# Kernel optimization log

Measured on AMD Instinct MI355X. Metric: run time of the kernel, lower is better.

The kernel has to match this reference:

```python
import jax, jax.numpy as jnp
import numpy as np

N = 50000   # nodes
E = 600000  # edges (avg degree ~12)
R = 8       # num_relations = 2 * n_speakers**2, n_speakers=2
B = 32      # num_bases = args.batch_size
GD, H1, H2 = 128, 128, 128


def setup_inputs() -> dict:
    key = jax.random.key(0)
    ks = jax.random.split(key, 16)
    w = lambda k, shape: jax.random.normal(k, shape, jnp.float32) * 0.05
    return {
        "node_features": jax.random.normal(ks[0], (N, GD), jnp.float32),
        "edge_index": jax.random.randint(ks[1], (2, E), 0, N),
        "edge_norm": jax.random.uniform(ks[2], (E,), jnp.float32),
        "edge_type": jax.random.randint(ks[3], (E,), 0, R),
        "basis": w(ks[4], (B, GD, H1)),
        "comp": w(ks[5], (R, B)),
        "root": w(ks[6], (GD, H1)),
        "bias1": jnp.zeros((H1,), jnp.float32),
        "w_key": w(ks[7], (H1, H2)),
        "b_key": jnp.zeros((H2,), jnp.float32),
        "w_query": w(ks[8], (H1, H2)),
        "b_query": jnp.zeros((H2,), jnp.float32),
        "w_value": w(ks[9], (H1, H2)),
        "b_value": jnp.zeros((H2,), jnp.float32),
        "w_skip": w(ks[10], (H1, H2)),
        "b_skip": jnp.zeros((H2,), jnp.float32),
    }


def reference(node_features, edge_index, edge_norm, edge_type, basis, comp,
              root, bias1, w_key, b_key, w_query, b_query, w_value, b_value,
              w_skip, b_skip):
    n = node_features.shape[0]
    r = comp.shape[0]
    src, dst = edge_index[0], edge_index[1]

    # ---- RGCNConv (basis decomposition, per-relation mean aggregation) ----
    W = jnp.einsum('rb,bio->rio', comp, basis)            # [R, GD, H1]
    xW = jnp.einsum('ni,rio->rno', node_features, W)      # [R, N, H1]
    msg = xW[edge_type, src]                              # [E, H1]
    seg = edge_type * n + dst                             # combined (relation, dst) segment id
    agg = jax.ops.segment_sum(msg, seg, num_segments=r * n).reshape(r, n, -1)
    cnt = jax.ops.segment_sum(jnp.ones(msg.shape[0], jnp.float32), seg,
                              num_segments=r * n).reshape(r, n, 1)
    h = (agg / jnp.maximum(cnt, 1.0)).sum(0) + node_features @ root + bias1

    # ---- ResGatedGraphConv: sigmoid(k_i + q_j) * v_j, sum-aggregated + skip ----
    k = h @ w_key + b_key
    q = h @ w_query + b_query
    v = h @ w_value + b_value
    m = jax.nn.sigmoid(k[dst] + q[src]) * v[src]          # [E, H2]
    out = jax.ops.segment_sum(m, dst, num_segments=n) + h @ w_skip + b_skip
    return out
```

## Files before the change

kernel.cpp:

```cpp
#include <hip/hip_runtime.h>
#include <stdint.h>

#define GD 128
#define H1 128
#define H2 128
#define NBASES 32
#define NREL 8
#define KA 1152

typedef __attribute__((ext_vector_type(8))) short bf16x8;
typedef __attribute__((ext_vector_type(4))) float f32x4;

static inline size_t align256(size_t x){ return (x + 255) & ~(size_t)255; }

__device__ __forceinline__ float bf2f(uint32_t u16){
  union { uint32_t u; float f; } c; c.u = (u16 & 0xffffu) << 16; return c.f;
}
__device__ __forceinline__ unsigned short f2bf(float f){
  union { float f; uint32_t u; } c; c.f = f;
  uint32_t u = c.u;
  u += 0x7fffu + ((u >> 16) & 1u);
  return (unsigned short)(u >> 16);
}
__device__ __forceinline__ uint32_t pkbf(float a, float b){
  union { float f; uint32_t u; } ca, cb; ca.f = a; cb.f = b;
  return __builtin_amdgcn_perm(cb.u + 0x8000u, ca.u + 0x8000u, 0x07060302u);
}

__device__ __forceinline__ void async_copy16(void* lds_dst, const void* gsrc){
  __builtin_amdgcn_global_load_lds(
      (const __attribute__((address_space(1))) uint32_t*)gsrc,
      (__attribute__((address_space(3))) uint32_t*)lds_dst, 16, 0, 0);
}

__global__ void k_prep(const float* __restrict__ comp, const float* __restrict__ basis,
                       const float* __restrict__ root, unsigned short* __restrict__ Bht,
                       const float* __restrict__ wk, const float* __restrict__ wq,
                       const float* __restrict__ wv, const float* __restrict__ wsk,
                       const float* __restrict__ bk, const float* __restrict__ bq,
                       const float* __restrict__ bv, const float* __restrict__ bs,
                       unsigned short* __restrict__ B2t, float* __restrict__ Bb,
                       const float4* __restrict__ x, uint2* __restrict__ xout, int cnt4,
                       const int* __restrict__ edst, const int* __restrict__ etyp,
                       int* __restrict__ cnt, int E, int n){
  const float LOG2E = 1.4426950408889634f;
  int b = blockIdx.x, t = threadIdx.x;
  if (b < 576){
    int idx = b*256 + t;
    int row = idx >> 7, i = idx & 127;
    int r = row >> 7, o = row & 127;
    float v;
    if (r < 8){
      float acc = 0.f;
      #pragma unroll
      for (int bb = 0; bb < NBASES; ++bb)
        acc += comp[r*NBASES + bb] * basis[((size_t)bb*GD + i)*H1 + o];
      v = acc;
    } else {
      v = root[(size_t)i*H1 + o];
    }
    Bht[(size_t)o*KA + r*128 + i] = f2bf(v);
  } else if (b < 576 + 256){
    int idx = (b - 576)*256 + t;
    int c = idx / H1, k = idx % H1;
    const float* w = (c < 128) ? wk : (c < 256) ? wq : (c < 384) ? wv : wsk;
    float val = w[(size_t)k*H2 + (c & 127)];
    if (c < 256) val *= LOG2E;
    B2t[idx] = f2bf(val);
    if (idx < 512){
      const float* bia = (idx < 128) ? bk : (idx < 256) ? bq : (idx < 384) ? bv : bs;
      float bval = bia[idx & 127];
      if (idx < 256) bval *= LOG2E;
      Bb[idx] = bval;
    }
  } else {
    int cb = b - (576 + 256);
    int ncastb = (cnt4 + 255) >> 8;
    if (cb < ncastb){
      int i = cb*256 + t;
      if (i < cnt4){
        float4 v = x[i];
        uint2 o; o.x = pkbf(v.x, v.y); o.y = pkbf(v.z, v.w);
        xout[i] = o;
      }
    } else {
      int e = (cb - ncastb)*256 + t;
      if (e < E) atomicAdd(&cnt[etyp[e]*n + edst[e]], 1);
    }
  }
}

__global__ void k_scanA(const int* __restrict__ deg, int* __restrict__ off,
                        int* __restrict__ btot, int len){
  __shared__ int wsum[16];
  int t = threadIdx.x, lane = t & 63, w = t >> 6;
  int i0 = blockIdx.x*8192 + t*8;
  int v[8];
  if (i0 + 7 < len){
    int4 va = *(const int4*)(deg + i0);
    int4 vb = *(const int4*)(deg + i0 + 4);
    v[0]=va.x; v[1]=va.y; v[2]=va.z; v[3]=va.w;
    v[4]=vb.x; v[5]=vb.y; v[6]=vb.z; v[7]=vb.w;
  } else {
    #pragma unroll
    for (int u = 0; u < 8; ++u) v[u] = (i0+u < len) ? deg[i0+u] : 0;
  }
  int s[8]; s[0] = v[0];
  #pragma unroll
  for (int u = 1; u < 8; ++u) s[u] = s[u-1] + v[u];
  int x = s[7];
  #pragma unroll
  for (int d = 1; d < 64; d <<= 1){
    int u = __shfl_up(x, d, 64);
    if (lane >= d) x += u;
  }
  if (lane == 63) wsum[w] = x;
  __syncthreads();
  if (t < 16){
    int y = wsum[t];
    #pragma unroll
    for (int d = 1; d < 16; d <<= 1){
      int u = __shfl_up(y, d, 16);
      if (t >= d) y += u;
    }
    wsum[t] = y;
  }
  __syncthreads();
  int woff = (w > 0) ? wsum[w-1] : 0;
  int excl = woff + x - s[7];
  #pragma unroll
  for (int u = 0; u < 8; ++u)
    if (i0+u < len) off[i0+u] = excl + s[u] - v[u];
  if (t == 0) btot[blockIdx.x] = wsum[15];
}

__global__ void k_scanB(const int* __restrict__ btot, int* __restrict__ off,
                        int* __restrict__ cursor, int len, int sentinel){
  int t = threadIdx.x, bid = blockIdx.x;
  int add = 0;
  for (int j = 0; j < bid; ++j) add += btot[j];
  int i0 = bid*8192 + t*8;
  #pragma unroll
  for (int u = 0; u < 8; ++u){
    int i = i0 + u;
    if (i < len){ int val = off[i] + add; off[i] = val; cursor[i] = val; }
  }
  if (bid == 0 && t == 0) off[len] = sentinel;
}

__global__ void k_scatter_rd(const int* __restrict__ src, const int* __restrict__ dst,
                             const int* __restrict__ typ, int* __restrict__ cursor,
                             int* __restrict__ pk, int E, int n){
  int e = blockIdx.x*blockDim.x + threadIdx.x;
  if (e >= E) return;
  int pos = atomicAdd(&cursor[typ[e]*n + dst[e]], 1);
  pk[pos] = src[e];
}

__global__ void k_agg(const int* __restrict__ off_rd, const int* __restrict__ pk_rd,
                      const uint32_t* __restrict__ x32, unsigned short* __restrict__ A2,
                      int n, int npad){
  int wid = blockIdx.x*(blockDim.x >> 6) + (threadIdx.x >> 6);
  int lane = threadIdx.x & 63;
  if (wid >= npad) return;
  uint32_t* arow = (uint32_t*)(A2 + (size_t)wid*KA);
  if (wid >= n){
    #pragma unroll
    for (int u = 0; u < 9; ++u) arow[u*64 + lane] = 0u;
    return;
  }
  int r8 = lane & 7;
  int o_r = off_rd[(size_t)r8*n + wid];
  int e_r = off_rd[(size_t)r8*n + wid + 1];
  int c_r = e_r - o_r;
  int c0_ = __builtin_amdgcn_readlane(c_r, 0), c1_ = __builtin_amdgcn_readlane(c_r, 1);
  int c2_ = __builtin_amdgcn_readlane(c_r, 2), c3_ = __builtin_amdgcn_readlane(c_r, 3);
  int c4_ = __builtin_amdgcn_readlane(c_r, 4), c5_ = __builtin_amdgcn_readlane(c_r, 5);
  int c6_ = __builtin_amdgcn_readlane(c_r, 6), c7_ = __builtin_amdgcn_readlane(c_r, 7);
  int o0_ = __builtin_amdgcn_readlane(o_r, 0), o1_ = __builtin_amdgcn_readlane(o_r, 1);
  int o2_ = __builtin_amdgcn_readlane(o_r, 2), o3_ = __builtin_amdgcn_readlane(o_r, 3);
  int o4_ = __builtin_amdgcn_readlane(o_r, 4), o5_ = __builtin_amdgcn_readlane(o_r, 5);
  int o6_ = __builtin_amdgcn_readlane(o_r, 6), o7_ = __builtin_amdgcn_readlane(o_r, 7);

#define AGGR(rr, oo, cc)                                                        \
  {                                                                             \
    float a0 = 0.f, a1 = 0.f;                                                   \
    for (int jb = 0; jb < (cc); jb += 64){                                      \
      int m = (cc) - jb; if (m > 64) m = 64;                                    \
      int pj = (lane < m) ? pk_rd[(oo) + jb + lane] : 0;                        \
      int jj = 0;                                                               \
      for (; jj + 4 <= m; jj += 4){                                             \
        uint32_t g[4];                                                          \
        _Pragma("unroll")                                                       \
        for (int k = 0; k < 4; ++k){                                            \
          int sN = __builtin_amdgcn_readlane(pj, jj + k);                       \
          g[k] = x32[(size_t)(uint32_t)sN*64 + lane];                           \
        }                                                                       \
        _Pragma("unroll")                                                       \
        for (int k = 0; k < 4; ++k){ a0 += bf2f(g[k]); a1 += bf2f(g[k] >> 16); }\
      }                                                                         \
      for (; jj < m; ++jj){                                                     \
        int sN = __builtin_amdgcn_readlane(pj, jj);                             \
        uint32_t g = x32[(size_t)(uint32_t)sN*64 + lane];                       \
        a0 += bf2f(g); a1 += bf2f(g >> 16);                                     \
      }                                                                         \
    }                                                                           \
    float ic = ((cc) > 0) ? __builtin_amdgcn_rcpf((float)(cc)) : 0.f;           \
    arow[(rr)*64 + lane] = pkbf(a0*ic, a1*ic);                                  \
  }

  AGGR(0, o0_, c0_)
  AGGR(1, o1_, c1_)
  AGGR(2, o2_, c2_)
  AGGR(3, o3_, c3_)
  AGGR(4, o4_, c4_)
  AGGR(5, o5_, c5_)
  AGGR(6, o6_, c6_)
  AGGR(7, o7_, c7_)
#undef AGGR
  arow[512 + lane] = x32[(size_t)wid*64 + lane];
}

__launch_bounds__(256)
__global__ void k_hgemm(const unsigned short* __restrict__ A, const unsigned short* __restrict__ Bt,
                        const float* __restrict__ bias1, unsigned short* __restrict__ h){
  __shared__ char lds[16384];
  int t = threadIdx.x, lane = t & 63, wave = t >> 6;
  int row0 = blockIdx.x * 128;
  int mrow = lane & 15, quad = lane >> 4;
  int wrow = (wave & 1) * 64, wcol = (wave >> 1) * 64;
  int s = (mrow >> 1) & 3;

  const unsigned short* Asrc = A + (size_t)(row0 + (t >> 2))*KA + (((t & 3) ^ ((t >> 3) & 3)) << 3);
  const unsigned short* Bsrc = Bt + (size_t)(t >> 2)*KA + (((t & 3) ^ ((t >> 3) & 3)) << 3);
  char* ldsw = lds + wave*1024;

  int aoff = (wrow + mrow)*64 + ((quad ^ s) << 4);
  int boff = 8192 + (wcol + mrow)*64 + ((quad ^ s) << 4);

  f32x4 acc[4][4];
  #pragma unroll
  for (int i = 0; i < 4; ++i)
    #pragma unroll
    for (int j = 0; j < 4; ++j) acc[i][j] = (f32x4){0.f,0.f,0.f,0.f};

  for (int kt = 0; kt < KA; kt += 32){
    __syncthreads();
    async_copy16(ldsw,         Asrc + kt);
    async_copy16(ldsw + 4096,  Asrc + (size_t)64*KA + kt);
    async_copy16(ldsw + 8192,  Bsrc + kt);
    async_copy16(ldsw + 12288, Bsrc + (size_t)64*KA + kt);
    __syncthreads();
    bf16x8 af[4], bf[4];
    #pragma unroll
    for (int i = 0; i < 4; ++i) af[i] = *(const bf16x8*)(lds + aoff + i*1024);
    #pragma unroll
    for (int j = 0; j < 4; ++j) bf[j] = *(const bf16x8*)(lds + boff + j*1024);
    #pragma unroll
    for (int i = 0; i < 4; ++i)
      #pragma unroll
      for (int j = 0; j < 4; ++j)
        acc[i][j] = __builtin_amdgcn_mfma_f32_16x16x32_bf16(af[i], bf[j], acc[i][j], 0, 0, 0);
  }
  #pragma unroll
  for (int j = 0; j < 4; ++j){
    int col = wcol + j*16 + mrow;
    float bc = bias1[col];
    #pragma unroll
    for (int i = 0; i < 4; ++i)
      #pragma unroll
      for (int rg = 0; rg < 4; ++rg){
        int row = row0 + wrow + i*16 + quad*4 + rg;
        h[(size_t)row*H1 + col] = f2bf(acc[i][j][rg] + bc);
      }
  }
}

__launch_bounds__(256)
__global__ void k_gemm2(const unsigned short* __restrict__ A, const unsigned short* __restrict__ Bt,
                        const float* __restrict__ Bb, unsigned short* __restrict__ kqv,
                        unsigned short* __restrict__ skipb, int n){
  __shared__ char lds[16384];
  int t = threadIdx.x, lane = t & 63, wave = t >> 6;
  int row0 = blockIdx.x * 128;
  int c0 = blockIdx.y * 128;
  int mrow = lane & 15, quad = lane >> 4;
  int wrow = (wave & 1) * 64, wcol = (wave >> 1) * 64;
  int s = (mrow >> 1) & 3;

  const unsigned short* Asrc = A + (size_t)(row0 + (t >> 2))*H1 + (((t & 3) ^ ((t >> 3) & 3)) << 3);
  const unsigned short* Bsrc = Bt + (size_t)(c0 + (t >> 2))*H1 + (((t & 3) ^ ((t >> 3) & 3)) << 3);
  char* ldsw = lds + wave*1024;

  int aoff = (wrow + mrow)*64 + ((quad ^ s) << 4);
  int boff = 8192 + (wcol + mrow)*64 + ((quad ^ s) << 4);

  f32x4 acc[4][4];
  #pragma unroll
  for (int i = 0; i < 4; ++i)
    #pragma unroll
    for (int j = 0; j < 4; ++j) acc[i][j] = (f32x4){0.f,0.f,0.f,0.f};

  #pragma unroll
  for (int kt = 0; kt < H1; kt += 32){
    __syncthreads();
    async_copy16(ldsw,         Asrc + kt);
    async_copy16(ldsw + 4096,  Asrc + (size_t)64*H1 + kt);
    async_copy16(ldsw + 8192,  Bsrc + kt);
    async_copy16(ldsw + 12288, Bsrc + (size_t)64*H1 + kt);
    __syncthreads();
    bf16x8 af[4], bf[4];
    #pragma unroll
    for (int i = 0; i < 4; ++i) af[i] = *(const bf16x8*)(lds + aoff + i*1024);
    #pragma unroll
    for (int j = 0; j < 4; ++j) bf[j] = *(const bf16x8*)(lds + boff + j*1024);
    #pragma unroll
    for (int i = 0; i < 4; ++i)
      #pragma unroll
      for (int j = 0; j < 4; ++j)
        acc[i][j] = __builtin_amdgcn_mfma_f32_16x16x32_bf16(af[i], bf[j], acc[i][j], 0, 0, 0);
  }
  #pragma unroll
  for (int j = 0; j < 4; ++j){
    int col = c0 + wcol + j*16 + mrow;
    float bcol = Bb[col];
    #pragma unroll
    for (int i = 0; i < 4; ++i)
      #pragma unroll
      for (int rg = 0; rg < 4; ++rg){
        int rr = row0 + wrow + i*16 + quad*4 + rg;
        if (rr >= n) continue;
        float v = acc[i][j][rg] + bcol;
        if (col < 128){
          kqv[(size_t)rr*384 + col] = f2bf(v);
        } else if (col < 256){
          int jj = col - 128;
          kqv[(size_t)rr*384 + 128 + ((jj >> 1) << 2) + (jj & 1)] = f2bf(v);
        } else if (col < 384){
          int jj = col - 256;
          kqv[(size_t)rr*384 + 128 + ((jj >> 1) << 2) + 2 + (jj & 1)] = f2bf(v);
        } else {
          skipb[(size_t)rr*H2 + (col - 384)] = f2bf(v);
        }
      }
  }
}

__global__ void k_edge2(const int* __restrict__ off_rd, const int* __restrict__ pk_rd,
                        const unsigned short* __restrict__ kqv,
                        const unsigned short* __restrict__ skipb,
                        float* __restrict__ out, int n){
  int wid = blockIdx.x*(blockDim.x >> 6) + (threadIdx.x >> 6);
  int lane = threadIdx.x & 63;
  if (wid >= n) return;
  const uint32_t* kv32 = (const uint32_t*)kqv;
  int r = lane & 7;
  int o_r = off_rd[(size_t)r*n + wid];
  int e_r = off_rd[(size_t)r*n + wid + 1];
  int c_r = e_r - o_r;
  int c0_ = __builtin_amdgcn_readlane(c_r, 0), c1_ = __builtin_amdgcn_readlane(c_r, 1);
  int c2_ = __builtin_amdgcn_readlane(c_r, 2), c3_ = __builtin_amdgcn_readlane(c_r, 3);
  int c4_ = __builtin_amdgcn_readlane(c_r, 4), c5_ = __builtin_amdgcn_readlane(c_r, 5);
  int c6_ = __builtin_amdgcn_readlane(c_r, 6), c7_ = __builtin_amdgcn_readlane(c_r, 7);
  int o0_ = __builtin_amdgcn_readlane(o_r, 0), o1_ = __builtin_amdgcn_readlane(o_r, 1);
  int o2_ = __builtin_amdgcn_readlane(o_r, 2), o3_ = __builtin_amdgcn_readlane(o_r, 3);
  int o4_ = __builtin_amdgcn_readlane(o_r, 4), o5_ = __builtin_amdgcn_readlane(o_r, 5);
  int o6_ = __builtin_amdgcn_readlane(o_r, 6), o7_ = __builtin_amdgcn_readlane(o_r, 7);
  int p1 = c0_, p2 = p1 + c1_, p3 = p2 + c2_, p4 = p3 + c3_;
  int p5 = p4 + c4_, p6 = p5 + c5_, p7 = p6 + c6_, dg = p7 + c7_;

  uint32_t ku = kv32[(size_t)wid*192 + lane];
  float k0 = bf2f(ku), k1 = bf2f(ku >> 16);
  float a0 = 0.f, a1 = 0.f;
  for (int jb = 0; jb < dg; jb += 64){
    int i = jb + lane;
    int adj = o0_;
    adj = (i >= p1) ? (o1_ - p1) : adj;
    adj = (i >= p2) ? (o2_ - p2) : adj;
    adj = (i >= p3) ? (o3_ - p3) : adj;
    adj = (i >= p4) ? (o4_ - p4) : adj;
    adj = (i >= p5) ? (o5_ - p5) : adj;
    adj = (i >= p6) ? (o6_ - p6) : adj;
    adj = (i >= p7) ? (o7_ - p7) : adj;
    int m = dg - jb; if (m > 64) m = 64;
    int pj = (lane < m) ? pk_rd[adj + i] : 0;
    int jj = 0;
    for (; jj + 8 <= m; jj += 8){
      uint2 q[8];
      #pragma unroll
      for (int k = 0; k < 8; ++k){
        int s = __builtin_amdgcn_readlane(pj, jj + k);
        q[k] = *(const uint2*)(kv32 + (size_t)s*192 + 64 + lane*2);
      }
      #pragma unroll
      for (int k = 0; k < 8; ++k){
        float qq0 = bf2f(q[k].x), qq1 = bf2f(q[k].x >> 16);
        float vv0 = bf2f(q[k].y), vv1 = bf2f(q[k].y >> 16);
        float g0 = __builtin_amdgcn_rcpf(1.f + __builtin_amdgcn_exp2f(-(k0 + qq0)));
        float g1 = __builtin_amdgcn_rcpf(1.f + __builtin_amdgcn_exp2f(-(k1 + qq1)));
        a0 += g0*vv0; a1 += g1*vv1;
      }
    }
    for (; jj + 4 <= m; jj += 4){
      uint2 q[4];
      #pragma unroll
      for (int k = 0; k < 4; ++k){
        int s = __builtin_amdgcn_readlane(pj, jj + k);
        q[k] = *(const uint2*)(kv32 + (size_t)s*192 + 64 + lane*2);
      }
      #pragma unroll
      for (int k = 0; k < 4; ++k){
        float qq0 = bf2f(q[k].x), qq1 = bf2f(q[k].x >> 16);
        float vv0 = bf2f(q[k].y), vv1 = bf2f(q[k].y >> 16);
        float g0 = __builtin_amdgcn_rcpf(1.f + __builtin_amdgcn_exp2f(-(k0 + qq0)));
        float g1 = __builtin_amdgcn_rcpf(1.f + __builtin_amdgcn_exp2f(-(k1 + qq1)));
        a0 += g0*vv0; a1 += g1*vv1;
      }
    }
    for (; jj < m; ++jj){
      int s = __builtin_amdgcn_readlane(pj, jj);
      uint2 qc = *(const uint2*)(kv32 + (size_t)s*192 + 64 + lane*2);
      float qq0 = bf2f(qc.x), qq1 = bf2f(qc.x >> 16);
      float vv0 = bf2f(qc.y), vv1 = bf2f(qc.y >> 16);
      float g0 = __builtin_amdgcn_rcpf(1.f + __builtin_amdgcn_exp2f(-(k0 + qq0)));
      float g1 = __builtin_amdgcn_rcpf(1.f + __builtin_amdgcn_exp2f(-(k1 + qq1)));
      a0 += g0*vv0; a1 += g1*vv1;
    }
  }
  uint32_t sk = ((const uint32_t*)skipb)[(size_t)wid*64 + lane];
  float2 cur; cur.x = a0 + bf2f(sk); cur.y = a1 + bf2f(sk >> 16);
  ((float2*)(out + (size_t)wid*H2))[lane] = cur;
}

extern "C" void kernel_launch(void* const* d_in, const int* in_sizes, int n_in,
                              void* d_out, int out_size, void* d_ws, size_t ws_size,
                              hipStream_t stream){
  const float* x     = (const float*)d_in[0];
  const int*   eidx  = (const int*)  d_in[1];
  const int*   etype = (const int*)  d_in[3];
  const float* basis = (const float*)d_in[4];
  const float* comp  = (const float*)d_in[5];
  const float* root  = (const float*)d_in[6];
  const float* bias1 = (const float*)d_in[7];
  const float* wk    = (const float*)d_in[8];
  const float* bk    = (const float*)d_in[9];
  const float* wq    = (const float*)d_in[10];
  const float* bq    = (const float*)d_in[11];
  const float* wv    = (const float*)d_in[12];
  const float* bv    = (const float*)d_in[13];
  const float* wsk   = (const float*)d_in[14];
  const float* bs    = (const float*)d_in[15];
  const int n = in_sizes[0] / GD;
  const int E = in_sizes[3];
  const int npad = (n + 127) & ~127;
  const int* esrc = eidx;
  const int* edst = eidx + E;
  float* out = (float*)d_out;

  char* w = (char*)d_ws;
  size_t off = 0;
  unsigned short* xbf  = (unsigned short*)(w + off); off = align256(off + (size_t)npad*GD*2);
  unsigned short* A2   = (unsigned short*)(w + off); off = align256(off + (size_t)npad*KA*2);
  unsigned short* Bht  = (unsigned short*)(w + off); off = align256(off + (size_t)KA*H1*2);
  unsigned short* B2t  = (unsigned short*)(w + off); off = align256(off + (size_t)512*H1*2);
  float* Bb            = (float*)(w + off);          off = align256(off + 512*4);
  unsigned short* hbuf = (unsigned short*)(w + off); off = align256(off + (size_t)npad*H1*2);
  unsigned short* kqv  = (unsigned short*)(w + off); off = align256(off + (size_t)n*384*2);
  unsigned short* skipb= (unsigned short*)(w + off); off = align256(off + (size_t)npad*H2*2);
  int* cnt_rd          = (int*)(w + off);            off = align256(off + (size_t)(8*n+4)*4);
  int* off_rd          = (int*)(w + off);            off = align256(off + (size_t)(8*n+1)*4);
  int* cur_rd          = (int*)(w + off);            off = align256(off + (size_t)8*n*4);
  int* btot_rd         = (int*)(w + off);            off = align256(off + 64*4);
  int* pk_rd           = (int*)(w + off);            off = align256(off + (size_t)E*4);

  const int nblk_rd = (8*n + 8191) / 8192;
  const int cnt4 = n*GD/4;
  const int ncastb = (cnt4 + 255)/256;
  const int histb  = (E + 255)/256;

  hipMemsetAsync(cnt_rd, 0, (size_t)8*n*4, stream);

  k_prep<<<576 + 256 + ncastb + histb, 256, 0, stream>>>(
      comp, basis, root, Bht, wk, wq, wv, wsk, bk, bq, bv, bs, B2t, Bb,
      (const float4*)x, (uint2*)xbf, cnt4,
      edst, etype, cnt_rd, E, n);
  k_scanA<<<nblk_rd, 1024, 0, stream>>>(cnt_rd, off_rd, btot_rd, 8*n);
  k_scanB<<<nblk_rd, 1024, 0, stream>>>(btot_rd, off_rd, cur_rd, 8*n, E);
  k_scatter_rd<<<(E + 255)/256, 256, 0, stream>>>(esrc, edst, etype, cur_rd, pk_rd, E, n);
  k_agg<<<(npad + 3)/4, 256, 0, stream>>>(off_rd, pk_rd, (const uint32_t*)xbf, A2, n, npad);
  k_hgemm<<<npad/128, 256, 0, stream>>>(A2, Bht, bias1, hbuf);
  k_gemm2<<<dim3(npad/128, 4), 256, 0, stream>>>(hbuf, B2t, Bb, kqv, skipb, n);
  k_edge2<<<(n + 3)/4, 256, 0, stream>>>(off_rd, pk_rd, kqv, skipb, out, n);
}
```

Measured before the change: 391.6 us.

## Merge per-relation aggregation loops and read root features directly in GEMM

The aggregation kernel now walks all eight relations' neighbor lists as one concatenated stream per node. It batches eight gathers at a time and flushes the running sum at relation boundaries, instead of running eight short, poorly unrolled loops. The A2 buffer drops its copied root-feature slice (1024 columns instead of 1152). The hgemm kernel instead reads the last K-chunk straight from the bf16 feature buffer, whose pad rows are now zeroed in the prep kernel. This cuts redundant writes and reads and improves gather latency hiding, at the cost of more per-element branching for the flush logic.

```diff
diff --git a/kernel.cpp b/kernel.cpp
--- a/kernel.cpp
+++ b/kernel.cpp
@@ -41,6 +41,7 @@
                        const float* __restrict__ bv, const float* __restrict__ bs,
                        unsigned short* __restrict__ B2t, float* __restrict__ Bb,
                        const float4* __restrict__ x, uint2* __restrict__ xout, int cnt4,
+                       uint32_t* __restrict__ xpadz, int npadz,
                        const int* __restrict__ edst, const int* __restrict__ etyp,
                        int* __restrict__ cnt, int E, int n){
   const float LOG2E = 1.4426950408889634f;
@@ -83,8 +84,11 @@
         uint2 o; o.x = pkbf(v.x, v.y); o.y = pkbf(v.z, v.w);
         xout[i] = o;
       }
+    } else if (cb < ncastb + 12){
+      int i = (cb - ncastb)*256 + t;
+      if (i < npadz) xpadz[i] = 0u;
     } else {
-      int e = (cb - ncastb)*256 + t;
+      int e = (cb - ncastb - 12)*256 + t;
       if (e < E) atomicAdd(&cnt[etyp[e]*n + edst[e]], 1);
     }
   }
@@ -163,16 +167,17 @@
   int wid = blockIdx.x*(blockDim.x >> 6) + (threadIdx.x >> 6);
   int lane = threadIdx.x & 63;
   if (wid >= npad) return;
-  uint32_t* arow = (uint32_t*)(A2 + (size_t)wid*KA);
+  uint32_t* arow = (uint32_t*)(A2 + (size_t)wid*1024);
   if (wid >= n){
     #pragma unroll
-    for (int u = 0; u < 9; ++u) arow[u*64 + lane] = 0u;
+    for (int u = 0; u < 8; ++u) arow[u*64 + lane] = 0u;
     return;
   }
   int r8 = lane & 7;
   int o_r = off_rd[(size_t)r8*n + wid];
   int e_r = off_rd[(size_t)r8*n + wid + 1];
   int c_r = e_r - o_r;
+  float ic_r = (c_r > 0) ? __builtin_amdgcn_rcpf((float)c_r) : 0.f;
   int c0_ = __builtin_amdgcn_readlane(c_r, 0), c1_ = __builtin_amdgcn_readlane(c_r, 1);
   int c2_ = __builtin_amdgcn_readlane(c_r, 2), c3_ = __builtin_amdgcn_readlane(c_r, 3);
   int c4_ = __builtin_amdgcn_readlane(c_r, 4), c5_ = __builtin_amdgcn_readlane(c_r, 5);
@@ -181,48 +186,74 @@
   int o2_ = __builtin_amdgcn_readlane(o_r, 2), o3_ = __builtin_amdgcn_readlane(o_r, 3);
   int o4_ = __builtin_amdgcn_readlane(o_r, 4), o5_ = __builtin_amdgcn_readlane(o_r, 5);
   int o6_ = __builtin_amdgcn_readlane(o_r, 6), o7_ = __builtin_amdgcn_readlane(o_r, 7);
-
-#define AGGR(rr, oo, cc)                                                        \
+  int p1 = c0_, p2 = p1 + c1_, p3 = p2 + c2_, p4 = p3 + c3_;
+  int p5 = p4 + c4_, p6 = p5 + c5_, p7 = p6 + c6_, dg = p7 + c7_;
+
+  int cr = 0;
+  float a0 = 0.f, a1 = 0.f;
+
+#define FLUSH(RK)                                                               \
   {                                                                             \
-    float a0 = 0.f, a1 = 0.f;                                                   \
-    for (int jb = 0; jb < (cc); jb += 64){                                      \
-      int m = (cc) - jb; if (m > 64) m = 64;                                    \
-      int pj = (lane < m) ? pk_rd[(oo) + jb + lane] : 0;                        \
-      int jj = 0;                                                               \
-      for (; jj + 4 <= m; jj += 4){                                             \
-        uint32_t g[4];                                                          \
-        _Pragma("unroll")                                                       \
-        for (int k = 0; k < 4; ++k){                                            \
-          int sN = __builtin_amdgcn_readlane(pj, jj + k);                       \
-          g[k] = x32[(size_t)(uint32_t)sN*64 + lane];                           \
-        }                                                                       \
-        _Pragma("unroll")                                                       \
-        for (int k = 0; k < 4; ++k){ a0 += bf2f(g[k]); a1 += bf2f(g[k] >> 16); }\
-      }                                                                         \
-      for (; jj < m; ++jj){                                                     \
-        int sN = __builtin_amdgcn_readlane(pj, jj);                             \
-        uint32_t g = x32[(size_t)(uint32_t)sN*64 + lane];                       \
-        a0 += bf2f(g); a1 += bf2f(g >> 16);                                     \
-      }                                                                         \
-    }                                                                           \
-    float ic = ((cc) > 0) ? __builtin_amdgcn_rcpf((float)(cc)) : 0.f;           \
-    arow[(rr)*64 + lane] = pkbf(a0*ic, a1*ic);                                  \
-  }
-
-  AGGR(0, o0_, c0_)
-  AGGR(1, o1_, c1_)
-  AGGR(2, o2_, c2_)
-  AGGR(3, o3_, c3_)
-  AGGR(4, o4_, c4_)
-  AGGR(5, o5_, c5_)
-  AGGR(6, o6_, c6_)
-  AGGR(7, o7_, c7_)
-#undef AGGR
-  arow[512 + lane] = x32[(size_t)wid*64 + lane];
+    float ic = __int_as_float(__builtin_amdgcn_readlane(__float_as_int(ic_r), cr)); \
+    arow[cr*64 + lane] = pkbf(a0*ic, a1*ic);                                    \
+    for (int q = cr + 1; q < (RK); ++q) arow[q*64 + lane] = 0u;                 \
+    cr = (RK); a0 = 0.f; a1 = 0.f;                                              \
+  }
+
+  for (int jb = 0; jb < dg; jb += 64){
+    int i = jb + lane;
+    int adj = o0_, rel = 0;
+    adj = (i >= p1) ? (o1_ - p1) : adj;  rel += (i >= p1);
+    adj = (i >= p2) ? (o2_ - p2) : adj;  rel += (i >= p2);
+    adj = (i >= p3) ? (o3_ - p3) : adj;  rel += (i >= p3);
+    adj = (i >= p4) ? (o4_ - p4) : adj;  rel += (i >= p4);
+    adj = (i >= p5) ? (o5_ - p5) : adj;  rel += (i >= p5);
+    adj = (i >= p6) ? (o6_ - p6) : adj;  rel += (i >= p6);
+    adj = (i >= p7) ? (o7_ - p7) : adj;  rel += (i >= p7);
+    int m = dg - jb; if (m > 64) m = 64;
+    int pj = (lane < m) ? pk_rd[adj + i] : 0;
+    int jj = 0;
+    for (; jj + 8 <= m; jj += 8){
+      uint32_t g[8];
+      #pragma unroll
+      for (int k = 0; k < 8; ++k){
+        int sN = __builtin_amdgcn_readlane(pj, jj + k);
+        g[k] = x32[(size_t)(uint32_t)sN*64 + lane];
+      }
+      #pragma unroll
+      for (int k = 0; k < 8; ++k){
+        int rk = __builtin_amdgcn_readlane(rel, jj + k);
+        if (rk != cr) FLUSH(rk);
+        a0 += bf2f(g[k]); a1 += bf2f(g[k] >> 16);
+      }
+    }
+    for (; jj < m; jj += 4){
+      int lim = m - 1;
+      uint32_t g[4];
+      #pragma unroll
+      for (int k = 0; k < 4; ++k){
+        int tt = jj + k; if (tt > lim) tt = lim;
+        int sN = __builtin_amdgcn_readlane(pj, tt);
+        g[k] = x32[(size_t)(uint32_t)sN*64 + lane];
+      }
+      #pragma unroll
+      for (int k = 0; k < 4; ++k){
+        int tt = jj + k;
+        if (tt < m){
+          int rk = __builtin_amdgcn_readlane(rel, tt);
+          if (rk != cr) FLUSH(rk);
+          a0 += bf2f(g[k]); a1 += bf2f(g[k] >> 16);
+        }
+      }
+    }
+  }
+  FLUSH(8)
+#undef FLUSH
 }
 
 __launch_bounds__(256)
-__global__ void k_hgemm(const unsigned short* __restrict__ A, const unsigned short* __restrict__ Bt,
+__global__ void k_hgemm(const unsigned short* __restrict__ A, const unsigned short* __restrict__ xb,
+                        const unsigned short* __restrict__ Bt,
                         const float* __restrict__ bias1, unsigned short* __restrict__ h){
   __shared__ char lds[16384];
   int t = threadIdx.x, lane = t & 63, wave = t >> 6;
@@ -230,9 +261,11 @@
   int mrow = lane & 15, quad = lane >> 4;
   int wrow = (wave & 1) * 64, wcol = (wave >> 1) * 64;
   int s = (mrow >> 1) & 3;
-
-  const unsigned short* Asrc = A + (size_t)(row0 + (t >> 2))*KA + (((t & 3) ^ ((t >> 3) & 3)) << 3);
-  const unsigned short* Bsrc = Bt + (size_t)(t >> 2)*KA + (((t & 3) ^ ((t >> 3) & 3)) << 3);
+  int colsw = (((t & 3) ^ ((t >> 3) & 3)) << 3);
+
+  const unsigned short* Asrc = A  + (size_t)(row0 + (t >> 2))*1024 + colsw;
+  const unsigned short* Xsrc = xb + (size_t)(row0 + (t >> 2))*GD   + colsw;
+  const unsigned short* Bsrc = Bt + (size_t)(t >> 2)*KA + colsw;
   char* ldsw = lds + wave*1024;
 
   int aoff = (wrow + mrow)*64 + ((quad ^ s) << 4);
@@ -245,9 +278,13 @@
     for (int j = 0; j < 4; ++j) acc[i][j] = (f32x4){0.f,0.f,0.f,0.f};
 
   for (int kt = 0; kt < KA; kt += 32){
+    const unsigned short* a0p = (kt < 1024) ? (Asrc + kt)
+                                            : (Xsrc + (kt - 1024));
+    const unsigned short* a1p = (kt < 1024) ? (Asrc + (size_t)64*1024 + kt)
+                                            : (Xsrc + (size_t)64*GD + (kt - 1024));
     __syncthreads();
-    async_copy16(ldsw,         Asrc + kt);
-    async_copy16(ldsw + 4096,  Asrc + (size_t)64*KA + kt);
+    async_copy16(ldsw,         a0p);
+    async_copy16(ldsw + 4096,  a1p);
     async_copy16(ldsw + 8192,  Bsrc + kt);
     async_copy16(ldsw + 12288, Bsrc + (size_t)64*KA + kt);
     __syncthreads();
@@ -460,7 +497,7 @@
   char* w = (char*)d_ws;
   size_t off = 0;
   unsigned short* xbf  = (unsigned short*)(w + off); off = align256(off + (size_t)npad*GD*2);
-  unsigned short* A2   = (unsigned short*)(w + off); off = align256(off + (size_t)npad*KA*2);
+  unsigned short* A2   = (unsigned short*)(w + off); off = align256(off + (size_t)npad*1024*2);
   unsigned short* Bht  = (unsigned short*)(w + off); off = align256(off + (size_t)KA*H1*2);
   unsigned short* B2t  = (unsigned short*)(w + off); off = align256(off + (size_t)512*H1*2);
   float* Bb            = (float*)(w + off);          off = align256(off + 512*4);
@@ -477,18 +514,20 @@
   const int cnt4 = n*GD/4;
   const int ncastb = (cnt4 + 255)/256;
   const int histb  = (E + 255)/256;
+  const int npadz  = (npad - n)*GD/2;
 
   hipMemsetAsync(cnt_rd, 0, (size_t)8*n*4, stream);
 
-  k_prep<<<576 + 256 + ncastb + histb, 256, 0, stream>>>(
+  k_prep<<<576 + 256 + ncastb + 12 + histb, 256, 0, stream>>>(
       comp, basis, root, Bht, wk, wq, wv, wsk, bk, bq, bv, bs, B2t, Bb,
       (const float4*)x, (uint2*)xbf, cnt4,
+      (uint32_t*)(xbf + (size_t)n*GD), npadz,
       edst, etype, cnt_rd, E, n);
   k_scanA<<<nblk_rd, 1024, 0, stream>>>(cnt_rd, off_rd, btot_rd, 8*n);
   k_scanB<<<nblk_rd, 1024, 0, stream>>>(btot_rd, off_rd, cur_rd, 8*n, E);
   k_scatter_rd<<<(E + 255)/256, 256, 0, stream>>>(esrc, edst, etype, cur_rd, pk_rd, E, n);
   k_agg<<<(npad + 3)/4, 256, 0, stream>>>(off_rd, pk_rd, (const uint32_t*)xbf, A2, n, npad);
-  k_hgemm<<<npad/128, 256, 0, stream>>>(A2, Bht, bias1, hbuf);
+  k_hgemm<<<npad/128, 256, 0, stream>>>(A2, xbf, Bht, bias1, hbuf);
   k_gemm2<<<dim3(npad/128, 4), 256, 0, stream>>>(hbuf, B2t, Bb, kqv, skipb, n);
   k_edge2<<<(n + 3)/4, 256, 0, stream>>>(off_rd, pk_rd, kqv, skipb, out, n);
 }
```

After: 365.7 us. 6.6% less time.
